# Optimization experiments

Hardware: AMD Instinct MI355X
Metric: run time of the kernel (lower is better)

## Reference

```python
import jax, jax.numpy as jnp
import numpy as np
import math

D_MODEL = 512
D_STATE = 16
D_CONV = 4
EXPAND = 2
D_INNER = D_MODEL * EXPAND
B, L = 2, 2048
EPS = 1e-8


def setup_inputs() -> dict:
    key = jax.random.key(0)
    ks = jax.random.split(key, 10)
    s_in = 1.0 / math.sqrt(D_MODEL)
    s_x = 1.0 / math.sqrt(D_INNER)
    s_c = 1.0 / math.sqrt(D_CONV)
    return {
        "x": jax.random.normal(ks[0], (B, L, D_MODEL), jnp.float32),
        "W_in": jax.random.uniform(ks[1], (D_MODEL, 2 * D_INNER), jnp.float32, -s_in, s_in),
        "b_in": jax.random.uniform(ks[2], (2 * D_INNER,), jnp.float32, -s_in, s_in),
        "conv_w": jax.random.uniform(ks[3], (D_INNER, 1, D_CONV), jnp.float32, -s_c, s_c),
        "conv_b": jax.random.uniform(ks[4], (D_INNER,), jnp.float32, -s_c, s_c),
        "W_x": jax.random.uniform(ks[5], (D_INNER, 2 * D_STATE + 1), jnp.float32, -s_x, s_x),
        "b_x": jax.random.uniform(ks[6], (2 * D_STATE + 1,), jnp.float32, -s_x, s_x),
        "A_log": jax.random.uniform(ks[7], (D_STATE,), jnp.float32, -math.log(D_STATE), -1.0),
        "D": jnp.ones((D_INNER,), jnp.float32),
        "W_out": jax.random.uniform(ks[8], (D_INNER, D_MODEL), jnp.float32, -s_x, s_x),
        "b_out": jax.random.uniform(ks[9], (D_MODEL,), jnp.float32, -s_x, s_x),
    }


def _silu(v):
    return v * jax.nn.sigmoid(v)


def _causal_depthwise_conv(x_blc, conv_w, conv_b):
    # x_blc: (B, L, D_inner); conv_w: (D_inner, 1, K). Torch pads K-1 both sides
    # then slices [:L] == causal left pad of K-1.
    lhs = jnp.transpose(x_blc, (0, 2, 1))  # (B, C, L)
    out = jax.lax.conv_general_dilated(
        lhs, conv_w,
        window_strides=(1,),
        padding=[(D_CONV - 1, 0)],
        dimension_numbers=("NCH", "OIH", "NCH"),
        feature_group_count=D_INNER,
    )
    out = out + conv_b[None, :, None]
    return jnp.transpose(out, (0, 2, 1))  # (B, L, C)


def reference(x, W_in, b_in, conv_w, conv_b, W_x, b_x, A_log, D, W_out, b_out):
    # in_proj and split
    xr = x @ W_in + b_in                      # (B, L, 2*Di)
    x_inner, res = jnp.split(xr, 2, axis=-1)  # each (B, L, Di)

    xc = _silu(_causal_depthwise_conv(x_inner, conv_w, conv_b))  # (B, L, Di)

    # selective scan (cumprod/cumsum formulation, faithful to source)
    BCdt = xc @ W_x + b_x                     # (B, L, 2S+1)
    B_sel = BCdt[..., :D_STATE]               # (B, L, S)
    C_sel = BCdt[..., D_STATE:2 * D_STATE]    # (B, L, S)
    dt = jax.nn.softplus(BCdt[..., -1:])      # (B, L, 1)

    A = -jnp.exp(A_log)                       # (S,)
    A_bar = jnp.exp(dt * A[None, None, :])    # (B, L, S)
    P = jnp.maximum(jnp.cumprod(A_bar, axis=1), EPS)  # (B, L, S)

    u = B_sel[..., None] * xc[:, :, None, :]  # (B, L, S, Di)
    g = jnp.cumsum(u / P[..., None], axis=1)  # (B, L, S, Di)
    h = g * P[..., None]                      # (B, L, S, Di)
    y = jnp.einsum("bls,blsd->bld", C_sel, h) + D[None, None, :] * xc

    y = y * _silu(res)
    return y @ W_out + b_out
```

## Files before the change

### kernel.cpp

```cpp
#include <hip/hip_runtime.h>
#include <hip/hip_bf16.h>
#include <cmath>


#define L_SEQ 2048
#define NBATCH 2
#define DI 1024
#define NC 64
#define LC 32
#define EPS_F 1e-8f
#define LOG_EPS -18.420680744f

typedef __attribute__((ext_vector_type(8))) __bf16 bf16x8;
typedef __attribute__((ext_vector_type(4))) float f32x4;

__device__ __forceinline__ float silu_f(float v) {
    return v / (1.f + __expf(-v));
}

__device__ __forceinline__ ushort bf16_bits(float v) {
    __hip_bfloat16 h = __float2bfloat16(v);
    return *reinterpret_cast<ushort*>(&h);
}

__device__ __forceinline__ float bf2f(ushort u) {
    union { unsigned u; float f; } c;
    c.u = ((unsigned)u) << 16;
    return c.f;
}

__device__ __forceinline__ float rate_of(float A, float dl, float cl, float cp) {
    if (A * cl >= LOG_EPS) return __expf(A * dl);
    float lp = A * cp;
    return (lp >= LOG_EPS) ? EPS_F / __expf(lp) : 1.f;
}

__global__ __launch_bounds__(256) void gemm1_mfma(
    const ushort* __restrict__ A, const ushort* __restrict__ Bt,
    const float* __restrict__ bias, ushort* __restrict__ C0,
    ushort* __restrict__ C1, int M, int N, int K)
{
    __shared__ ushort lA[128 * 64];
    __shared__ ushort lB[128 * 64];
    const int tid = threadIdx.x;
    const int w = tid >> 6, ln = tid & 63;
    const int wr = w >> 1, wc = w & 1;
    const int bm = blockIdx.y * 128, bn = blockIdx.x * 128;
    const int q = ln >> 4, r = ln & 15;
    f32x4 acc[4][4] = {};

    for (int k0 = 0; k0 < K; k0 += 64) {
        #pragma unroll
        for (int j = 0; j < 4; ++j) {
            int i = (w * 4 + j) * 64 + ln;
            int m = i >> 3, k8 = (i & 7) * 8;
            __builtin_amdgcn_global_load_lds(
                (const __attribute__((address_space(1))) void*)(A + (size_t)(bm + m) * K + k0 + k8),
                (__attribute__((address_space(3))) void*)(lA + (size_t)i * 8),
                16, 0, 0);
            __builtin_amdgcn_global_load_lds(
                (const __attribute__((address_space(1))) void*)(Bt + (size_t)(bn + m) * K + k0 + k8),
                (__attribute__((address_space(3))) void*)(lB + (size_t)i * 8),
                16, 0, 0);
        }
        __syncthreads();
        #pragma unroll
        for (int kk = 0; kk < 2; ++kk) {
            const int ko = kk * 32 + q * 8;
            bf16x8 af[4], bfr[4];
            #pragma unroll
            for (int m = 0; m < 4; ++m)
                af[m] = *reinterpret_cast<const bf16x8*>(&lA[(wr * 64 + m * 16 + r) * 64 + ko]);
            #pragma unroll
            for (int n = 0; n < 4; ++n)
                bfr[n] = *reinterpret_cast<const bf16x8*>(&lB[(wc * 64 + n * 16 + r) * 64 + ko]);
            #pragma unroll
            for (int m = 0; m < 4; ++m)
                #pragma unroll
                for (int n = 0; n < 4; ++n)
                    acc[m][n] = __builtin_amdgcn_mfma_f32_16x16x32_bf16(af[m], bfr[n], acc[m][n], 0, 0, 0);
        }
        __syncthreads();
    }

    const bool lo = (bn < 1024);
    #pragma unroll
    for (int n = 0; n < 4; ++n) {
        int col = bn + wc * 64 + n * 16 + r;
        float bv = bias[col];
        #pragma unroll
        for (int m = 0; m < 4; ++m) {
            int row0 = bm + wr * 64 + m * 16 + q * 4;
            #pragma unroll
            for (int j = 0; j < 4; ++j) {
                ushort v = bf16_bits(acc[m][n][j] + bv);
                if (lo) C0[(size_t)(row0 + j) * 1024 + col] = v;
                else    C1[(size_t)(row0 + j) * 1024 + (col - 1024)] = v;
            }
        }
    }
}

__global__ __launch_bounds__(256) void gemm2_mfma(
    const ushort* __restrict__ A, const ushort* __restrict__ Bt,
    const float* __restrict__ bias, float* __restrict__ C,
    int M, int N, int K)
{
    __shared__ ushort lA[128 * 64];
    __shared__ ushort lB[64 * 64];
    const int tid = threadIdx.x;
    const int w = tid >> 6, ln = tid & 63;
    const int wr = w >> 1, wc = w & 1;
    const int bm = blockIdx.y * 128, bn = blockIdx.x * 64;
    const int q = ln >> 4, r = ln & 15;
    f32x4 acc[4][2] = {};

    for (int k0 = 0; k0 < K; k0 += 64) {
        #pragma unroll
        for (int j = 0; j < 4; ++j) {
            int i = (w * 4 + j) * 64 + ln;
            int m = i >> 3, k8 = (i & 7) * 8;
            __builtin_amdgcn_global_load_lds(
                (const __attribute__((address_space(1))) void*)(A + (size_t)(bm + m) * K + k0 + k8),
                (__attribute__((address_space(3))) void*)(lA + (size_t)i * 8),
                16, 0, 0);
        }
        #pragma unroll
        for (int j = 0; j < 2; ++j) {
            int i = (w * 2 + j) * 64 + ln;
            int m = i >> 3, k8 = (i & 7) * 8;
            __builtin_amdgcn_global_load_lds(
                (const __attribute__((address_space(1))) void*)(Bt + (size_t)(bn + m) * K + k0 + k8),
                (__attribute__((address_space(3))) void*)(lB + (size_t)i * 8),
                16, 0, 0);
        }
        __syncthreads();
        #pragma unroll
        for (int kk = 0; kk < 2; ++kk) {
            const int ko = kk * 32 + q * 8;
            bf16x8 af[4], bfr[2];
            #pragma unroll
            for (int m = 0; m < 4; ++m)
                af[m] = *reinterpret_cast<const bf16x8*>(&lA[(wr * 64 + m * 16 + r) * 64 + ko]);
            #pragma unroll
            for (int n = 0; n < 2; ++n)
                bfr[n] = *reinterpret_cast<const bf16x8*>(&lB[(wc * 32 + n * 16 + r) * 64 + ko]);
            #pragma unroll
            for (int m = 0; m < 4; ++m)
                #pragma unroll
                for (int n = 0; n < 2; ++n)
                    acc[m][n] = __builtin_amdgcn_mfma_f32_16x16x32_bf16(af[m], bfr[n], acc[m][n], 0, 0, 0);
        }
        __syncthreads();
    }

    #pragma unroll
    for (int n = 0; n < 2; ++n) {
        int col = bn + wc * 32 + n * 16 + r;
        float bv = bias[col];
        #pragma unroll
        for (int m = 0; m < 4; ++m) {
            int row0 = bm + wr * 64 + m * 16 + q * 4;
            #pragma unroll
            for (int j = 0; j < 4; ++j)
                C[(size_t)(row0 + j) * N + col] = acc[m][n][j] + bv;
        }
    }
}

__global__ __launch_bounds__(256) void conv_gemm3(
    const ushort* __restrict__ xinb, const float* __restrict__ cw,
    const float* __restrict__ cb, const ushort* __restrict__ Wxt,
    ushort* __restrict__ xcb, float* __restrict__ P)
{
    __shared__ ushort sxin[67 * 128];
    __shared__ ushort sxc[64 * 128];
    __shared__ ushort swx[48 * 128];
    __shared__ float  scw[128][4];
    __shared__ float  scb[128];

    const int t = threadIdx.x;
    const int ks = blockIdx.x, rt = blockIdx.y;
    const int bm = rt * 64;
    const int kb = ks * 128;
    const int l0 = bm & (L_SEQ - 1);

    for (int i = t; i < 67 * 16; i += 256) {
        int rr = i >> 4, c8 = (i & 15) * 8;
        uint4 v = {0, 0, 0, 0};
        if (l0 + rr - 3 >= 0)
            v = *reinterpret_cast<const uint4*>(&xinb[(size_t)(bm + rr - 3) * 1024 + kb + c8]);
        *reinterpret_cast<uint4*>(&sxin[rr * 128 + c8]) = v;
    }
    for (int i = t; i < 48 * 16; i += 256) {
        int rr = i >> 4, c8 = (i & 15) * 8;
        *reinterpret_cast<uint4*>(&swx[rr * 128 + c8]) =
            *reinterpret_cast<const uint4*>(&Wxt[(size_t)rr * 1024 + kb + c8]);
    }
    for (int i = t; i < 512; i += 256) scw[i >> 2][i & 3] = cw[(size_t)(kb + (i >> 2)) * 4 + (i & 3)];
    if (t < 128) scb[t] = cb[kb + t];
    __syncthreads();

    for (int i = t; i < 1024; i += 256) {
        int row = i >> 4, c8 = (i & 15) * 8;
        ushort ov[8];
        #pragma unroll
        for (int j = 0; j < 8; ++j) {
            int col = c8 + j;
            float a = scb[col];
            a = fmaf(bf2f(sxin[(row + 0) * 128 + col]), scw[col][0], a);
            a = fmaf(bf2f(sxin[(row + 1) * 128 + col]), scw[col][1], a);
            a = fmaf(bf2f(sxin[(row + 2) * 128 + col]), scw[col][2], a);
            a = fmaf(bf2f(sxin[(row + 3) * 128 + col]), scw[col][3], a);
            ov[j] = bf16_bits(silu_f(a));
        }
        *reinterpret_cast<uint4*>(&sxc[row * 128 + c8]) = *reinterpret_cast<uint4*>(ov);
        *reinterpret_cast<uint4*>(&xcb[(size_t)(bm + row) * 1024 + kb + c8]) =
            *reinterpret_cast<uint4*>(ov);
    }
    __syncthreads();

    const int w = t >> 6, ln = t & 63;
    const int q = ln >> 4, r = ln & 15;
    f32x4 acc[3] = {};
    #pragma unroll
    for (int kk = 0; kk < 4; ++kk) {
        const int ko = kk * 32 + q * 8;
        bf16x8 af = *reinterpret_cast<const bf16x8*>(&sxc[(w * 16 + r) * 128 + ko]);
        #pragma unroll
        for (int n = 0; n < 3; ++n) {
            bf16x8 bf = *reinterpret_cast<const bf16x8*>(&swx[(n * 16 + r) * 128 + ko]);
            acc[n] = __builtin_amdgcn_mfma_f32_16x16x32_bf16(af, bf, acc[n], 0, 0, 0);
        }
    }

    const int row0 = bm + w * 16 + q * 4;
    const size_t base = (size_t)ks * 196608;
    #pragma unroll
    for (int n = 0; n < 3; ++n)
        #pragma unroll
        for (int j = 0; j < 4; ++j)
            P[base + (size_t)(row0 + j) * 48 + n * 16 + r] = acc[n][j];
}

__global__ __launch_bounds__(256) void gemm3_reduce(
    const float* __restrict__ P, const float* __restrict__ b_x,
    float* __restrict__ scal32, float* __restrict__ dtr)
{
    const int bid = blockIdx.x;
    if (bid < 512) {
        int idx = bid * 256 + threadIdx.x;
        int l = idx >> 5, c = idx & 31;
        int pi = l * 48 + c;
        float v = b_x[c];
        #pragma unroll
        for (int k = 0; k < 8; ++k) v += P[pi + k * 196608];
        scal32[idx] = v;
    } else {
        int l = (bid - 512) * 256 + threadIdx.x;
        int pi = l * 48 + 32;
        float v = b_x[32];
        #pragma unroll
        for (int k = 0; k < 8; ++k) v += P[pi + k * 196608];
        dtr[l] = v;
    }
}

__global__ __launch_bounds__(256) void prep_all(
    const float* __restrict__ x, const float* __restrict__ W_in,
    const float* __restrict__ W_out, const float* __restrict__ W_x,
    ushort* __restrict__ xbf, ushort* __restrict__ Wt1,
    ushort* __restrict__ Wt2, ushort* __restrict__ Wxt)
{
    const int bid = blockIdx.x;
    const int t = threadIdx.x;
    if (bid < 2048) {
        int i = bid * 256 + t;
        float4 v = reinterpret_cast<const float4*>(x)[i];
        ushort4 o;
        o.x = bf16_bits(v.x); o.y = bf16_bits(v.y);
        o.z = bf16_bits(v.z); o.w = bf16_bits(v.w);
        reinterpret_cast<ushort4*>(xbf)[i] = o;
        return;
    }
    if (bid >= 2432) {
        int idx = (bid - 2432) * 256 + t;
        int c = idx >> 10, k = idx & 1023;
        Wxt[idx] = (c < 33) ? bf16_bits(W_x[(size_t)k * 33 + c]) : (ushort)0;
        return;
    }
    __shared__ float ld[64][65];
    const float* src; ushort* dst; int R, C, tile;
    if (bid < 2304) { src = W_in;  dst = Wt1; R = 512;  C = 2048; tile = bid - 2048; }
    else            { src = W_out; dst = Wt2; R = 1024; C = 512;  tile = bid - 2304; }
    const int ctiles = C / 64;
    const int r0 = (tile / ctiles) * 64, c0 = (tile % ctiles) * 64;
    #pragma unroll
    for (int i = 0; i < 16; ++i) {
        int idx = t + i * 256;
        int rr = idx >> 6, cc = idx & 63;
        ld[rr][cc] = src[(size_t)(r0 + rr) * C + c0 + cc];
    }
    __syncthreads();
    #pragma unroll
    for (int i = 0; i < 16; ++i) {
        int idx = t + i * 256;
        int cc = idx >> 6, rr = idx & 63;
        dst[(size_t)(c0 + cc) * R + r0 + rr] = bf16_bits(ld[rr][cc]);
    }
}

__global__ __launch_bounds__(256) void rates_scan(
    const float* __restrict__ dtr, const float* __restrict__ A_log,
    float* __restrict__ dtv, float* __restrict__ dtc, float* __restrict__ RP)
{
    int b = blockIdx.x;
    int t = threadIdx.x;
    __shared__ float cdt[L_SEQ];
    __shared__ float wsum[4];
    __shared__ float An[16];
    if (t < 16) An[t] = -__expf(A_log[t]);
    const float* dr = dtr + (size_t)b * L_SEQ;

    float dt[8];
    float run = 0.f;
    const int l0 = t * 8;
    #pragma unroll
    for (int i = 0; i < 8; ++i) {
        float raw = dr[l0 + i];
        float d = (raw > 20.f) ? raw : log1pf(__expf(raw));
        dt[i] = d;
        run += d;
        cdt[l0 + i] = run;
    }

    float x = run;
    int lane = t & 63;
    #pragma unroll
    for (int d = 1; d < 64; d <<= 1) {
        float v = __shfl_up(x, d, 64);
        if (lane >= d) x += v;
    }
    int w = t >> 6;
    if (lane == 63) wsum[w] = x;
    __syncthreads();
    float woff = 0.f;
    for (int i = 0; i < w; ++i) woff += wsum[i];
    float toff = woff + x - run;
    #pragma unroll
    for (int i = 0; i < 8; ++i) cdt[l0 + i] += toff;
    __syncthreads();

    float cv[8];
    #pragma unroll
    for (int i = 0; i < 8; ++i) cv[i] = cdt[l0 + i];
    float4* dv = reinterpret_cast<float4*>(dtv + (size_t)b * L_SEQ + l0);
    float4* dc = reinterpret_cast<float4*>(dtc + (size_t)b * L_SEQ + l0);
    dv[0] = *reinterpret_cast<float4*>(&dt[0]);
    dv[1] = *reinterpret_cast<float4*>(&dt[4]);
    dc[0] = *reinterpret_cast<float4*>(&cv[0]);
    dc[1] = *reinterpret_cast<float4*>(&cv[4]);

    if ((t & 3) == 3) {
        int c = t >> 2;
        float ce = cdt[c * LC + LC - 1];
        float cp = (c == 0) ? 0.f : cdt[c * LC - 1];
        for (int s = 0; s < 16; ++s) {
            float A = An[s];
            float pe = fmaxf(__expf(A * ce), EPS_F);
            float pp = fmaxf(__expf(A * cp), EPS_F);
            RP[(b * NC + c) * 16 + s] = pe / pp;
        }
    }
}

__global__ __launch_bounds__(128) void scan_states(
    const float* __restrict__ scal32, const float* __restrict__ dtv,
    const float* __restrict__ dtc, const float* __restrict__ A_log,
    const ushort* __restrict__ xcb, ushort* __restrict__ Sbf)
{
    int b = blockIdx.z, c = blockIdx.y;
    int d = blockIdx.x * 128 + threadIdx.x;
    const int t = threadIdx.x;
    __shared__ float sbc[LC * 32];
    __shared__ float srt[LC][16];
    __shared__ float An[16];

    const float4* src = reinterpret_cast<const float4*>(scal32 + ((size_t)(b * L_SEQ) + c * LC) * 32);
    float4* dst = reinterpret_cast<float4*>(sbc);
    for (int i = t; i < LC * 32 / 4; i += 128) dst[i] = src[i];
    if (t < 16) An[t] = -__expf(A_log[t]);

    const ushort* xcp = xcb + ((size_t)(b * L_SEQ) + c * LC) * 1024 + d;
    float xv[LC];
    #pragma unroll
    for (int ll = 0; ll < LC; ++ll) xv[ll] = bf2f(xcp[(size_t)ll * 1024]);
    __syncthreads();

    {
        const int gb = b * L_SEQ + c * LC;
        #pragma unroll
        for (int k = 0; k < 4; ++k) {
            int idx = t * 4 + k;
            int l = idx >> 4, s = idx & 15;
            float cl = dtc[gb + l];
            float dl = dtv[gb + l];
            float cp = (c == 0 && l == 0) ? 0.f : dtc[gb + l - 1];
            srt[l][s] = rate_of(An[s], dl, cl, cp);
        }
    }
    __syncthreads();

    float h[16];
    #pragma unroll
    for (int s = 0; s < 16; ++s) h[s] = 0.f;
    #pragma unroll
    for (int ll = 0; ll < LC; ++ll) {
        const float* e = sbc + ll * 32;
        #pragma unroll
        for (int s = 0; s < 16; ++s) h[s] = fmaf(srt[ll][s], h[s], e[s] * xv[ll]);
    }
    ushort* Sp = Sbf + ((size_t)(b * NC + c) * 16) * 1024 + d;
    #pragma unroll
    for (int s = 0; s < 16; ++s) Sp[(size_t)s * 1024] = bf16_bits(h[s]);
}

__global__ __launch_bounds__(256) void stitch(
    ushort* __restrict__ Sbf, const float* __restrict__ RP)
{
    const int tid = threadIdx.x;
    const int idx = blockIdx.x * 256 + tid;
    const int b = blockIdx.y;
    const int d = idx & 1023, s = idx >> 10;
    __shared__ float rps[NC];
    if (tid < NC) rps[tid] = RP[(b * NC + tid) * 16 + s];

    const long base = ((long)(b * NC) * 16 + s) * 1024 + d;
    const long cs = 16 * 1024;
    float v[NC];
    #pragma unroll
    for (int c = 0; c < NC; ++c) v[c] = bf2f(Sbf[base + c * cs]);
    __syncthreads();
    float H = 0.f;
    #pragma unroll
    for (int c = 0; c < NC; ++c) {
        float tmp = v[c];
        v[c] = H;
        H = fmaf(rps[c], H, tmp);
    }
    #pragma unroll
    for (int c = 0; c < NC; ++c) Sbf[base + c * cs] = bf16_bits(v[c]);
}

__global__ __launch_bounds__(128) void scan_out(
    const float* __restrict__ scal32, const float* __restrict__ dtv,
    const float* __restrict__ dtc, const float* __restrict__ A_log,
    const ushort* __restrict__ xcb, const ushort* __restrict__ Hin,
    const float* __restrict__ Dw, const ushort* __restrict__ resb,
    ushort* __restrict__ ybf)
{
    int b = blockIdx.z, c = blockIdx.y;
    int d = blockIdx.x * 128 + threadIdx.x;
    const int t = threadIdx.x;
    __shared__ float sbc[LC * 32];
    __shared__ float srt[LC][16];
    __shared__ float An[16];

    const float4* src = reinterpret_cast<const float4*>(scal32 + ((size_t)(b * L_SEQ) + c * LC) * 32);
    float4* dst = reinterpret_cast<float4*>(sbc);
    for (int i = t; i < LC * 32 / 4; i += 128) dst[i] = src[i];
    if (t < 16) An[t] = -__expf(A_log[t]);

    const long row0 = (long)(b * L_SEQ) + c * LC;
    float xv[LC], rv[LC];
    #pragma unroll
    for (int ll = 0; ll < LC; ++ll) xv[ll] = bf2f(xcb[(row0 + ll) * 1024 + d]);
    #pragma unroll
    for (int ll = 0; ll < LC; ++ll) rv[ll] = bf2f(resb[(row0 + ll) * 1024 + d]);
    float h[16];
    long hoff = ((long)(b * NC + c) * 16) * 1024 + d;
    #pragma unroll
    for (int s = 0; s < 16; ++s) h[s] = bf2f(Hin[hoff + (long)s * 1024]);
    __syncthreads();

    {
        const int gb = b * L_SEQ + c * LC;
        #pragma unroll
        for (int k = 0; k < 4; ++k) {
            int idx = t * 4 + k;
            int l = idx >> 4, s = idx & 15;
            float cl = dtc[gb + l];
            float dl = dtv[gb + l];
            float cp = (c == 0 && l == 0) ? 0.f : dtc[gb + l - 1];
            srt[l][s] = rate_of(An[s], dl, cl, cp);
        }
    }
    __syncthreads();

    float Dd = Dw[d];
    #pragma unroll
    for (int ll = 0; ll < LC; ++ll) {
        const float* e = sbc + ll * 32;
        float y = 0.f;
        #pragma unroll
        for (int s = 0; s < 16; ++s) {
            h[s] = fmaf(srt[ll][s], h[s], e[s] * xv[ll]);
            y = fmaf(e[16 + s], h[s], y);
        }
        y = fmaf(Dd, xv[ll], y);
        ybf[(row0 + ll) * 1024 + d] = bf16_bits(y * silu_f(rv[ll]));
    }
}

extern "C" void kernel_launch(void* const* d_in, const int* in_sizes, int n_in,
                              void* d_out, int out_size, void* d_ws, size_t ws_size,
                              hipStream_t stream)
{
    const float* x      = (const float*)d_in[0];
    const float* W_in   = (const float*)d_in[1];
    const float* b_in   = (const float*)d_in[2];
    const float* conv_w = (const float*)d_in[3];
    const float* conv_b = (const float*)d_in[4];
    const float* W_x    = (const float*)d_in[5];
    const float* b_x    = (const float*)d_in[6];
    const float* A_log  = (const float*)d_in[7];
    const float* Dw     = (const float*)d_in[8];
    const float* W_out  = (const float*)d_in[9];
    const float* b_out  = (const float*)d_in[10];
    float* out = (float*)d_out;

    ushort* u    = (ushort*)d_ws;
    ushort* xinb = u;
    ushort* resb = xinb + 4194304;
    ushort* xcb  = resb + 4194304;
    ushort* Sbf  = xcb + 4194304;
    ushort* xbf  = Sbf + 2097152;
    ushort* Wt1  = xbf + 2097152;
    ushort* Wt2  = Wt1 + 1048576;
    ushort* Wxt  = Wt2 + 524288;
    ushort* ybf  = Wxt + 49152;
    float* scal32 = (float*)(ybf + 4194304);
    float* dtr   = scal32 + 131072;
    float* dtv   = dtr + 4096;
    float* dtc   = dtv + 4096;
    float* RP    = dtc + 4096;
    float* P     = RP + 2048;

    prep_all<<<2624, 256, 0, stream>>>(x, W_in, W_out, W_x, xbf, Wt1, Wt2, Wxt);

    gemm1_mfma<<<dim3(2048 / 128, 4096 / 128), 256, 0, stream>>>(
        xbf, Wt1, b_in, xinb, resb, 4096, 2048, 512);

    conv_gemm3<<<dim3(8, 64), 256, 0, stream>>>(xinb, conv_w, conv_b, Wxt, xcb, P);

    gemm3_reduce<<<528, 256, 0, stream>>>(P, b_x, scal32, dtr);

    rates_scan<<<NBATCH, 256, 0, stream>>>(dtr, A_log, dtv, dtc, RP);

    scan_states<<<dim3(DI / 128, NC, NBATCH), 128, 0, stream>>>(
        scal32, dtv, dtc, A_log, xcb, Sbf);
    stitch<<<dim3(64, NBATCH), 256, 0, stream>>>(Sbf, RP);
    scan_out<<<dim3(DI / 128, NC, NBATCH), 128, 0, stream>>>(
        scal32, dtv, dtc, A_log, xcb, Sbf, Dw, resb, ybf);

    gemm2_mfma<<<dim3(512 / 64, 4096 / 128), 256, 0, stream>>>(
        ybf, Wt2, b_out, out, 4096, 512, 1024);
}
```

Baseline: 102.2 us.

## Fold W_x/W_out weight prep into gemm1 launch and vectorize gemm3 reduce

Measured after the change: 102.6 us. About the same (+0.4%).

```diff
diff --git a/kernel.cpp b/kernel.cpp
--- a/kernel.cpp
+++ b/kernel.cpp
@@ -38,14 +38,44 @@
 __global__ __launch_bounds__(256) void gemm1_mfma(
     const ushort* __restrict__ A, const ushort* __restrict__ Bt,
     const float* __restrict__ bias, ushort* __restrict__ C0,
-    ushort* __restrict__ C1, int M, int N, int K)
+    ushort* __restrict__ C1, const float* __restrict__ W_x,
+    const float* __restrict__ W_out, ushort* __restrict__ Wxt,
+    ushort* __restrict__ Wt2, int K)
 {
     __shared__ ushort lA[128 * 64];
     __shared__ ushort lB[128 * 64];
+    const int bid = blockIdx.x;
     const int tid = threadIdx.x;
+
+    if (bid >= 512) {
+        if (bid < 704) {
+            int idx = (bid - 512) * 256 + tid;
+            int c = idx >> 10, k = idx & 1023;
+            Wxt[idx] = (c < 33) ? bf16_bits(W_x[(size_t)k * 33 + c]) : (ushort)0;
+        } else {
+            float* ld = reinterpret_cast<float*>(lA);
+            int tile = bid - 704;
+            int r0 = (tile >> 3) * 32, c0 = (tile & 7) * 64;
+            #pragma unroll
+            for (int i = 0; i < 8; ++i) {
+                int idx = tid + i * 256;
+                int rr = idx >> 6, cc = idx & 63;
+                ld[rr * 68 + cc] = W_out[(size_t)(r0 + rr) * 512 + c0 + cc];
+            }
+            __syncthreads();
+            #pragma unroll
+            for (int i = 0; i < 8; ++i) {
+                int idx = tid + i * 256;
+                int cc = idx >> 5, rr = idx & 31;
+                Wt2[(size_t)(c0 + cc) * 1024 + r0 + rr] = bf16_bits(ld[rr * 68 + cc]);
+            }
+        }
+        return;
+    }
+
     const int w = tid >> 6, ln = tid & 63;
     const int wr = w >> 1, wc = w & 1;
-    const int bm = blockIdx.y * 128, bn = blockIdx.x * 128;
+    const int bm = (bid >> 4) * 128, bn = (bid & 15) * 128;
     const int q = ln >> 4, r = ln & 15;
     f32x4 acc[4][4] = {};
 
@@ -248,16 +278,17 @@
     float* __restrict__ scal32, float* __restrict__ dtr)
 {
     const int bid = blockIdx.x;
-    if (bid < 512) {
+    if (bid < 128) {
         int idx = bid * 256 + threadIdx.x;
-        int l = idx >> 5, c = idx & 31;
-        int pi = l * 48 + c;
-        float v = b_x[c];
-        #pragma unroll
-        for (int k = 0; k < 8; ++k) v += P[pi + k * 196608];
-        scal32[idx] = v;
+        int l = idx >> 3, c4 = (idx & 7) * 4;
+        int pi = l * 48 + c4;
+        f32x4 v = *reinterpret_cast<const f32x4*>(&b_x[c4]);
+        #pragma unroll
+        for (int k = 0; k < 8; ++k)
+            v += *reinterpret_cast<const f32x4*>(&P[pi + k * 196608]);
+        *reinterpret_cast<f32x4*>(&scal32[(size_t)l * 32 + c4]) = v;
     } else {
-        int l = (bid - 512) * 256 + threadIdx.x;
+        int l = (bid - 128) * 256 + threadIdx.x;
         int pi = l * 48 + 32;
         float v = b_x[32];
         #pragma unroll
@@ -268,9 +299,7 @@
 
 __global__ __launch_bounds__(256) void prep_all(
     const float* __restrict__ x, const float* __restrict__ W_in,
-    const float* __restrict__ W_out, const float* __restrict__ W_x,
-    ushort* __restrict__ xbf, ushort* __restrict__ Wt1,
-    ushort* __restrict__ Wt2, ushort* __restrict__ Wxt)
+    ushort* __restrict__ xbf, ushort* __restrict__ Wt1)
 {
     const int bid = blockIdx.x;
     const int t = threadIdx.x;
@@ -283,30 +312,21 @@
         reinterpret_cast<ushort4*>(xbf)[i] = o;
         return;
     }
-    if (bid >= 2432) {
-        int idx = (bid - 2432) * 256 + t;
-        int c = idx >> 10, k = idx & 1023;
-        Wxt[idx] = (c < 33) ? bf16_bits(W_x[(size_t)k * 33 + c]) : (ushort)0;
-        return;
-    }
     __shared__ float ld[64][65];
-    const float* src; ushort* dst; int R, C, tile;
-    if (bid < 2304) { src = W_in;  dst = Wt1; R = 512;  C = 2048; tile = bid - 2048; }
-    else            { src = W_out; dst = Wt2; R = 1024; C = 512;  tile = bid - 2304; }
-    const int ctiles = C / 64;
-    const int r0 = (tile / ctiles) * 64, c0 = (tile % ctiles) * 64;
+    const int tile = bid - 2048;
+    const int r0 = (tile >> 5) * 64, c0 = (tile & 31) * 64;
     #pragma unroll
     for (int i = 0; i < 16; ++i) {
         int idx = t + i * 256;
         int rr = idx >> 6, cc = idx & 63;
-        ld[rr][cc] = src[(size_t)(r0 + rr) * C + c0 + cc];
+        ld[rr][cc] = W_in[(size_t)(r0 + rr) * 2048 + c0 + cc];
     }
     __syncthreads();
     #pragma unroll
     for (int i = 0; i < 16; ++i) {
         int idx = t + i * 256;
         int cc = idx >> 6, rr = idx & 63;
-        dst[(size_t)(c0 + cc) * R + r0 + rr] = bf16_bits(ld[rr][cc]);
+        Wt1[(size_t)(c0 + cc) * 512 + r0 + rr] = bf16_bits(ld[rr][cc]);
     }
 }
 
@@ -546,14 +566,14 @@
     float* RP    = dtc + 4096;
     float* P     = RP + 2048;
 
-    prep_all<<<2624, 256, 0, stream>>>(x, W_in, W_out, W_x, xbf, Wt1, Wt2, Wxt);
-
-    gemm1_mfma<<<dim3(2048 / 128, 4096 / 128), 256, 0, stream>>>(
-        xbf, Wt1, b_in, xinb, resb, 4096, 2048, 512);
+    prep_all<<<2304, 256, 0, stream>>>(x, W_in, xbf, Wt1);
+
+    gemm1_mfma<<<960, 256, 0, stream>>>(
+        xbf, Wt1, b_in, xinb, resb, W_x, W_out, Wxt, Wt2, 512);
 
     conv_gemm3<<<dim3(8, 64), 256, 0, stream>>>(xinb, conv_w, conv_b, Wxt, xcb, P);
 
-    gemm3_reduce<<<528, 256, 0, stream>>>(P, b_x, scal32, dtr);
+    gemm3_reduce<<<144, 256, 0, stream>>>(P, b_x, scal32, dtr);
 
     rates_scan<<<NBATCH, 256, 0, stream>>>(dtr, A_log, dtv, dtc, RP);
 
```
